# Optimization experiments

Hardware: AMD Instinct MI355X
Metric: run time of the kernel (lower is better)

## Reference

```python
import jax, jax.numpy as jnp
import numpy as np

B, T, D_IN, H, D_OUT = 4096, 512, 10, 20, 2


def setup_inputs() -> dict:
    key = jax.random.key(0)
    ks = jax.random.split(key, 12)
    s = 1.0 / np.sqrt(H)  # PyTorch-style uniform bound scale (use normal*s)
    return {
        "x": jax.random.normal(ks[0], (B, T, D_IN), jnp.float32),
        "w_ih0": jax.random.normal(ks[1], (H, D_IN), jnp.float32) * s,
        "w_hh0": jax.random.normal(ks[2], (H, H), jnp.float32) * s,
        "b_ih0": jax.random.normal(ks[3], (H,), jnp.float32) * s,
        "b_hh0": jax.random.normal(ks[4], (H,), jnp.float32) * s,
        "w_ih1": jax.random.normal(ks[5], (H, H), jnp.float32) * s,
        "w_hh1": jax.random.normal(ks[6], (H, H), jnp.float32) * s,
        "b_ih1": jax.random.normal(ks[7], (H,), jnp.float32) * s,
        "b_hh1": jax.random.normal(ks[8], (H,), jnp.float32) * s,
        "fc_w": jax.random.normal(ks[9], (D_OUT, H), jnp.float32) * s,
        "fc_b": jax.random.normal(ks[10], (D_OUT,), jnp.float32) * s,
    }


def _rnn_layer(inp, w_ih, w_hh, b_ih, b_hh):
    # inp: [B, T, Din]. Precompute input projection once (batched GEMM),
    # then scan the sequential recurrence: h_t = tanh(x_t W_ih^T + b_ih + h_{t-1} W_hh^T + b_hh)
    xp = jnp.einsum('btd,hd->bth', inp, w_ih) + (b_ih + b_hh)  # [B, T, H]

    def step(h, xt):
        h = jnp.tanh(xt + h @ w_hh.T)
        return h, h

    h0 = jnp.zeros((inp.shape[0], w_hh.shape[0]), inp.dtype)
    _, hs = jax.lax.scan(step, h0, jnp.swapaxes(xp, 0, 1))  # hs: [T, B, H]
    return jnp.swapaxes(hs, 0, 1)  # [B, T, H]


def reference(x, w_ih0, w_hh0, b_ih0, b_hh0, w_ih1, w_hh1, b_ih1, b_hh1, fc_w, fc_b):
    h1 = _rnn_layer(x, w_ih0, w_hh0, b_ih0, b_hh0)
    h2 = _rnn_layer(h1, w_ih1, w_hh1, b_ih1, b_hh1)
    last = h2[:, -1, :]  # [B, H]
    return last @ fc_w.T + fc_b  # [B, D_OUT]
```

## Files before the change

### kernel.cpp

```cpp
#include <hip/hip_runtime.h>
#include <cstdint>

constexpr int B_   = 4096;
constexpr int T_   = 512;
constexpr int DIN  = 10;
constexpr int H_   = 20;
constexpr int DOUT = 2;

constexpr int SPW = 3;
constexpr int CH  = 2;
constexpr int XV  = CH * DIN / 4;

typedef float    v2f __attribute__((ext_vector_type(2)));
typedef float    v4f __attribute__((ext_vector_type(4)));
typedef _Float16 h2t __attribute__((ext_vector_type(2)));

__device__ __forceinline__ v2f pkfma(v2f a, v2f b, v2f c) {
    return __builtin_elementwise_fma(a, b, c);
}

__device__ __forceinline__ float fdot2(h2t a, h2t b, float c) {
#if __has_builtin(__builtin_amdgcn_fdot2)
    return __builtin_amdgcn_fdot2(a, b, c, false);
#else
    return fmaf((float)a.x, (float)b.x, fmaf((float)a.y, (float)b.y, c));
#endif
}

__device__ __forceinline__ float fast_tanh(float v) {
    float e = __builtin_amdgcn_exp2f(v * 2.885390082f);
    float r = __builtin_amdgcn_rcpf(e + 1.0f);
    return fmaf(-2.0f, r, 1.0f);
}

union V4H { v4f f; h2t h[4]; };

extern "C" __global__ void __launch_bounds__(64, 1)
rnn_h16(const float* __restrict__ x,
        const float* __restrict__ w_ih0, const float* __restrict__ w_hh0,
        const float* __restrict__ b_ih0, const float* __restrict__ b_hh0,
        const float* __restrict__ w_ih1, const float* __restrict__ w_hh1,
        const float* __restrict__ b_ih1, const float* __restrict__ b_hh1,
        const float* __restrict__ fc_w, const float* __restrict__ fc_b,
        float* __restrict__ out)
{
    const int lane = threadIdx.x;
    const int sl   = lane / H_;
    const int i    = lane - sl * H_;
    const int samp = blockIdx.x * SPW + sl;
    const int sc   = (samp < B_) ? samp : (B_ - 1);
    const int slc  = (sl < SPW) ? sl : SPW;

    __shared__ __align__(16) _Float16 hs[SPW + 1][2 * H_];

    h2t wh0h[10], wi1h[10], wh1h[10];
    {
        const v4f* p0 = reinterpret_cast<const v4f*>(w_hh0 + i * H_);
        const v4f* p1 = reinterpret_cast<const v4f*>(w_ih1 + i * H_);
        const v4f* p2 = reinterpret_cast<const v4f*>(w_hh1 + i * H_);
        #pragma unroll
        for (int k = 0; k < 5; ++k) {
            v4f a = p0[k];
            wh0h[2*k]   = h2t{(_Float16)a.x, (_Float16)a.y};
            wh0h[2*k+1] = h2t{(_Float16)a.z, (_Float16)a.w};
            v4f b = p1[k];
            wi1h[2*k]   = h2t{(_Float16)b.x, (_Float16)b.y};
            wi1h[2*k+1] = h2t{(_Float16)b.z, (_Float16)b.w};
            v4f c = p2[k];
            wh1h[2*k]   = h2t{(_Float16)c.x, (_Float16)c.y};
            wh1h[2*k+1] = h2t{(_Float16)c.z, (_Float16)c.w};
        }
    }
    v2f wi0p[DIN / 2];
    {
        const v2f* p = reinterpret_cast<const v2f*>(w_ih0 + i * DIN);
        #pragma unroll
        for (int k = 0; k < DIN / 2; ++k) wi0p[k] = p[k];
    }
    const float bias0 = b_ih0[i] + b_hh0[i];
    const float bias1 = b_ih1[i] + b_hh1[i];

    h2t h1h[10], h2h[10];
    #pragma unroll
    for (int k = 0; k < 10; ++k) {
        h1h[k] = h2t{(_Float16)0.f, (_Float16)0.f};
        h2h[k] = h2t{(_Float16)0.f, (_Float16)0.f};
    }

    const v4f* xb = reinterpret_cast<const v4f*>(x + (size_t)sc * (T_ * DIN));

    v4f xv[XV];
    #pragma unroll
    for (int k = 0; k < XV; ++k) xv[k] = xb[k];

    auto getpair = [&](int p) -> v2f {
        v4f v = xv[p >> 1];
        return (p & 1) ? (v2f){v.z, v.w} : (v2f){v.x, v.y};
    };

    auto consume_xp = [&](float (&xp)[CH]) {
        #pragma unroll
        for (int m = 0; m < CH; ++m) {
            v2f acc = (v2f){bias0, 0.f};
            #pragma unroll
            for (int q = 0; q < DIN / 2; ++q)
                acc = pkfma(getpair(m * (DIN / 2) + q), wi0p[q], acc);
            xp[m] = acc.x + acc.y;
        }
    };

    auto row_read = [&]() {
        V4H r[5];
        #pragma unroll
        for (int k = 0; k < 5; ++k)
            r[k].f = reinterpret_cast<const v4f*>(&hs[slc][0])[k];
        #pragma unroll
        for (int k = 0; k < 2; ++k) {
            h1h[4*k+0] = r[k].h[0]; h1h[4*k+1] = r[k].h[1];
            h1h[4*k+2] = r[k].h[2]; h1h[4*k+3] = r[k].h[3];
        }
        h1h[8] = r[2].h[0]; h1h[9] = r[2].h[1];
        h2h[0] = r[2].h[2]; h2h[1] = r[2].h[3];
        #pragma unroll
        for (int k = 0; k < 2; ++k) {
            h2h[2+4*k+0] = r[3+k].h[0]; h2h[2+4*k+1] = r[3+k].h[1];
            h2h[2+4*k+2] = r[3+k].h[2]; h2h[2+4*k+3] = r[3+k].h[3];
        }
    };

    auto full_step = [&](float xpm) {
        float a0 = xpm, a1 = 0.f;
        #pragma unroll
        for (int k = 0; k < 5; ++k) {
            a0 = fdot2(h1h[2*k],   wh0h[2*k],   a0);
            a1 = fdot2(h1h[2*k+1], wh0h[2*k+1], a1);
        }
        float h1n = fast_tanh(a0 + a1);

        float b0 = bias1, b1 = 0.f;
        #pragma unroll
        for (int k = 0; k < 5; ++k) {
            b0 = fdot2(h1h[2*k],   wi1h[2*k],   b0);
            b1 = fdot2(h1h[2*k+1], wi1h[2*k+1], b1);
        }
        #pragma unroll
        for (int k = 0; k < 5; ++k) {
            b0 = fdot2(h2h[2*k],   wh1h[2*k],   b0);
            b1 = fdot2(h2h[2*k+1], wh1h[2*k+1], b1);
        }
        float h2n = fast_tanh(b0 + b1);

        hs[slc][i]      = (_Float16)h1n;
        hs[slc][H_ + i] = (_Float16)h2n;
        row_read();
    };

    {
        float xp[CH];
        consume_xp(xp);
        #pragma unroll
        for (int k = 0; k < XV; ++k) xv[k] = xb[(CH * DIN) / 4 + k];

        float h1n = fast_tanh(xp[0]);
        hs[slc][i]      = (_Float16)h1n;
        hs[slc][H_ + i] = (_Float16)0.f;
        row_read();

        #pragma unroll
        for (int m = 1; m < CH; ++m) full_step(xp[m]);
    }

    for (int t0 = CH; t0 < T_; t0 += CH) {
        float xp[CH];
        consume_xp(xp);
        {
            const int t0n = (t0 + CH < T_) ? (t0 + CH) : 0;
            #pragma unroll
            for (int k = 0; k < XV; ++k) xv[k] = xb[(t0n * DIN) / 4 + k];
        }
        #pragma unroll
        for (int m = 0; m < CH; ++m) full_step(xp[m]);
    }

    float h2fin[H_];
    {
        float b0 = bias1, b1 = 0.f;
        #pragma unroll
        for (int k = 0; k < 5; ++k) {
            b0 = fdot2(h1h[2*k],   wi1h[2*k],   b0);
            b1 = fdot2(h1h[2*k+1], wi1h[2*k+1], b1);
        }
        #pragma unroll
        for (int k = 0; k < 5; ++k) {
            b0 = fdot2(h2h[2*k],   wh1h[2*k],   b0);
            b1 = fdot2(h2h[2*k+1], wh1h[2*k+1], b1);
        }
        float h2n = fast_tanh(b0 + b1);
        hs[slc][H_ + i] = (_Float16)h2n;
        #pragma unroll
        for (int j = 0; j < H_; ++j) h2fin[j] = (float)hs[slc][H_ + j];
    }

    if (sl < SPW && samp < B_ && i < DOUT) {
        float acc = fc_b[i];
        #pragma unroll
        for (int j = 0; j < H_; ++j) acc = fmaf(h2fin[j], fc_w[i * H_ + j], acc);
        out[samp * DOUT + i] = acc;
    }
}

extern "C" void kernel_launch(void* const* d_in, const int* in_sizes, int n_in,
                              void* d_out, int out_size, void* d_ws, size_t ws_size,
                              hipStream_t stream) {
    (void)in_sizes; (void)n_in; (void)d_ws; (void)ws_size; (void)out_size;
    const float* x     = (const float*)d_in[0];
    const float* w_ih0 = (const float*)d_in[1];
    const float* w_hh0 = (const float*)d_in[2];
    const float* b_ih0 = (const float*)d_in[3];
    const float* b_hh0 = (const float*)d_in[4];
    const float* w_ih1 = (const float*)d_in[5];
    const float* w_hh1 = (const float*)d_in[6];
    const float* b_ih1 = (const float*)d_in[7];
    const float* b_hh1 = (const float*)d_in[8];
    const float* fc_w  = (const float*)d_in[9];
    const float* fc_b  = (const float*)d_in[10];
    float* out = (float*)d_out;

    const int grid = (B_ + SPW - 1) / SPW;
    hipLaunchKernelGGL(rnn_h16, dim3(grid), dim3(64), 0, stream,
                       x, w_ih0, w_hh0, b_ih0, b_hh0,
                       w_ih1, w_hh1, b_ih1, b_hh1, fc_w, fc_b, out);
}
```

Baseline: 136.7 us.

## Fold tanh scale into weights, split LDS row reads, widen dot accumulators

Pre-multiplies all weights and biases by 2/ln2 so the tanh needs no extra multiply on the serial path. The LDS row is padded to 48 halves so h1 and h2 get separate aligned reads. Layer-0's new h1 is written and read back before the layer-1 dot products run, which overlaps LDS latency with compute. The dependent dot-product chains now use four accumulators instead of two, which shortens the serial latency per step. Scaling the weights before the fp16 conversion slightly changes rounding and the fp16 range used.

```diff
diff --git a/kernel.cpp b/kernel.cpp
--- a/kernel.cpp
+++ b/kernel.cpp
@@ -10,10 +10,13 @@
 constexpr int SPW = 3;
 constexpr int CH  = 2;
 constexpr int XV  = CH * DIN / 4;
+constexpr int RS  = 48;
 
 typedef float    v2f __attribute__((ext_vector_type(2)));
 typedef float    v4f __attribute__((ext_vector_type(4)));
 typedef _Float16 h2t __attribute__((ext_vector_type(2)));
+
+constexpr float SCL = 2.885390082f;
 
 __device__ __forceinline__ v2f pkfma(v2f a, v2f b, v2f c) {
     return __builtin_elementwise_fma(a, b, c);
@@ -27,22 +30,23 @@
 #endif
 }
 
-__device__ __forceinline__ float fast_tanh(float v) {
-    float e = __builtin_amdgcn_exp2f(v * 2.885390082f);
+__device__ __forceinline__ float tanh_pre(float s) {
+    float e = __builtin_amdgcn_exp2f(s);
     float r = __builtin_amdgcn_rcpf(e + 1.0f);
     return fmaf(-2.0f, r, 1.0f);
 }
 
 union V4H { v4f f; h2t h[4]; };
+union V2H { v2f f; h2t h[2]; };
 
 extern "C" __global__ void __launch_bounds__(64, 1)
-rnn_h16(const float* __restrict__ x,
-        const float* __restrict__ w_ih0, const float* __restrict__ w_hh0,
-        const float* __restrict__ b_ih0, const float* __restrict__ b_hh0,
-        const float* __restrict__ w_ih1, const float* __restrict__ w_hh1,
-        const float* __restrict__ b_ih1, const float* __restrict__ b_hh1,
-        const float* __restrict__ fc_w, const float* __restrict__ fc_b,
-        float* __restrict__ out)
+rnn_h16b(const float* __restrict__ x,
+         const float* __restrict__ w_ih0, const float* __restrict__ w_hh0,
+         const float* __restrict__ b_ih0, const float* __restrict__ b_hh0,
+         const float* __restrict__ w_ih1, const float* __restrict__ w_hh1,
+         const float* __restrict__ b_ih1, const float* __restrict__ b_hh1,
+         const float* __restrict__ fc_w, const float* __restrict__ fc_b,
+         float* __restrict__ out)
 {
     const int lane = threadIdx.x;
     const int sl   = lane / H_;
@@ -51,7 +55,8 @@
     const int sc   = (samp < B_) ? samp : (B_ - 1);
     const int slc  = (sl < SPW) ? sl : SPW;
 
-    __shared__ __align__(16) _Float16 hs[SPW + 1][2 * H_];
+    __shared__ __align__(16) _Float16 hs[(SPW + 1) * RS];
+    _Float16* row = &hs[slc * RS];
 
     h2t wh0h[10], wi1h[10], wh1h[10];
     {
@@ -61,24 +66,27 @@
         #pragma unroll
         for (int k = 0; k < 5; ++k) {
             v4f a = p0[k];
-            wh0h[2*k]   = h2t{(_Float16)a.x, (_Float16)a.y};
-            wh0h[2*k+1] = h2t{(_Float16)a.z, (_Float16)a.w};
+            wh0h[2*k]   = h2t{(_Float16)(a.x*SCL), (_Float16)(a.y*SCL)};
+            wh0h[2*k+1] = h2t{(_Float16)(a.z*SCL), (_Float16)(a.w*SCL)};
             v4f b = p1[k];
-            wi1h[2*k]   = h2t{(_Float16)b.x, (_Float16)b.y};
-            wi1h[2*k+1] = h2t{(_Float16)b.z, (_Float16)b.w};
+            wi1h[2*k]   = h2t{(_Float16)(b.x*SCL), (_Float16)(b.y*SCL)};
+            wi1h[2*k+1] = h2t{(_Float16)(b.z*SCL), (_Float16)(b.w*SCL)};
             v4f c = p2[k];
-            wh1h[2*k]   = h2t{(_Float16)c.x, (_Float16)c.y};
-            wh1h[2*k+1] = h2t{(_Float16)c.z, (_Float16)c.w};
+            wh1h[2*k]   = h2t{(_Float16)(c.x*SCL), (_Float16)(c.y*SCL)};
+            wh1h[2*k+1] = h2t{(_Float16)(c.z*SCL), (_Float16)(c.w*SCL)};
         }
     }
     v2f wi0p[DIN / 2];
     {
         const v2f* p = reinterpret_cast<const v2f*>(w_ih0 + i * DIN);
         #pragma unroll
-        for (int k = 0; k < DIN / 2; ++k) wi0p[k] = p[k];
-    }
-    const float bias0 = b_ih0[i] + b_hh0[i];
-    const float bias1 = b_ih1[i] + b_hh1[i];
+        for (int k = 0; k < DIN / 2; ++k) {
+            v2f v = p[k];
+            wi0p[k] = (v2f){v.x * SCL, v.y * SCL};
+        }
+    }
+    const float bias0 = (b_ih0[i] + b_hh0[i]) * SCL;
+    const float bias1 = (b_ih1[i] + b_hh1[i]) * SCL;
 
     h2t h1h[10], h2h[10];
     #pragma unroll
@@ -109,50 +117,66 @@
         }
     };
 
-    auto row_read = [&]() {
-        V4H r[5];
-        #pragma unroll
-        for (int k = 0; k < 5; ++k)
-            r[k].f = reinterpret_cast<const v4f*>(&hs[slc][0])[k];
-        #pragma unroll
-        for (int k = 0; k < 2; ++k) {
-            h1h[4*k+0] = r[k].h[0]; h1h[4*k+1] = r[k].h[1];
-            h1h[4*k+2] = r[k].h[2]; h1h[4*k+3] = r[k].h[3];
-        }
-        h1h[8] = r[2].h[0]; h1h[9] = r[2].h[1];
-        h2h[0] = r[2].h[2]; h2h[1] = r[2].h[3];
-        #pragma unroll
-        for (int k = 0; k < 2; ++k) {
-            h2h[2+4*k+0] = r[3+k].h[0]; h2h[2+4*k+1] = r[3+k].h[1];
-            h2h[2+4*k+2] = r[3+k].h[2]; h2h[2+4*k+3] = r[3+k].h[3];
-        }
+    auto read_h1 = [&](V4H& r0, V4H& r1, V2H& r2) {
+        r0.f = *reinterpret_cast<const v4f*>(row + 0);
+        r1.f = *reinterpret_cast<const v4f*>(row + 8);
+        r2.f = *reinterpret_cast<const v2f*>(row + 16);
+    };
+    auto read_h2 = [&](V4H& r0, V4H& r1, V2H& r2) {
+        r0.f = *reinterpret_cast<const v4f*>(row + 24);
+        r1.f = *reinterpret_cast<const v4f*>(row + 32);
+        r2.f = *reinterpret_cast<const v2f*>(row + 40);
+    };
+    auto commit = [&](h2t (&dst)[10], const V4H& r0, const V4H& r1, const V2H& r2) {
+        dst[0]=r0.h[0]; dst[1]=r0.h[1]; dst[2]=r0.h[2]; dst[3]=r0.h[3];
+        dst[4]=r1.h[0]; dst[5]=r1.h[1]; dst[6]=r1.h[2]; dst[7]=r1.h[3];
+        dst[8]=r2.h[0]; dst[9]=r2.h[1];
     };
 
     auto full_step = [&](float xpm) {
-        float a0 = xpm, a1 = 0.f;
-        #pragma unroll
-        for (int k = 0; k < 5; ++k) {
-            a0 = fdot2(h1h[2*k],   wh0h[2*k],   a0);
-            a1 = fdot2(h1h[2*k+1], wh0h[2*k+1], a1);
-        }
-        float h1n = fast_tanh(a0 + a1);
-
-        float b0 = bias1, b1 = 0.f;
-        #pragma unroll
-        for (int k = 0; k < 5; ++k) {
-            b0 = fdot2(h1h[2*k],   wi1h[2*k],   b0);
-            b1 = fdot2(h1h[2*k+1], wi1h[2*k+1], b1);
-        }
-        #pragma unroll
-        for (int k = 0; k < 5; ++k) {
-            b0 = fdot2(h2h[2*k],   wh1h[2*k],   b0);
-            b1 = fdot2(h2h[2*k+1], wh1h[2*k+1], b1);
-        }
-        float h2n = fast_tanh(b0 + b1);
-
-        hs[slc][i]      = (_Float16)h1n;
-        hs[slc][H_ + i] = (_Float16)h2n;
-        row_read();
+        float a0 = xpm, a1 = 0.f, a2 = 0.f, a3 = 0.f;
+        #pragma unroll
+        for (int k = 0; k < 8; k += 4) {
+            a0 = fdot2(h1h[k+0], wh0h[k+0], a0);
+            a1 = fdot2(h1h[k+1], wh0h[k+1], a1);
+            a2 = fdot2(h1h[k+2], wh0h[k+2], a2);
+            a3 = fdot2(h1h[k+3], wh0h[k+3], a3);
+        }
+        a0 = fdot2(h1h[8], wh0h[8], a0);
+        a1 = fdot2(h1h[9], wh0h[9], a1);
+        float h1n = tanh_pre((a0 + a1) + (a2 + a3));
+
+        row[i] = (_Float16)h1n;
+        V4H n10, n11; V2H n12;
+        read_h1(n10, n11, n12);
+
+        float b0 = bias1, b1 = 0.f, b2 = 0.f, b3 = 0.f;
+        #pragma unroll
+        for (int k = 0; k < 8; k += 4) {
+            b0 = fdot2(h1h[k+0], wi1h[k+0], b0);
+            b1 = fdot2(h1h[k+1], wi1h[k+1], b1);
+            b2 = fdot2(h1h[k+2], wi1h[k+2], b2);
+            b3 = fdot2(h1h[k+3], wi1h[k+3], b3);
+        }
+        b0 = fdot2(h1h[8], wi1h[8], b0);
+        b1 = fdot2(h1h[9], wi1h[9], b1);
+        #pragma unroll
+        for (int k = 0; k < 8; k += 4) {
+            b2 = fdot2(h2h[k+0], wh1h[k+0], b2);
+            b3 = fdot2(h2h[k+1], wh1h[k+1], b3);
+            b0 = fdot2(h2h[k+2], wh1h[k+2], b0);
+            b1 = fdot2(h2h[k+3], wh1h[k+3], b1);
+        }
+        b2 = fdot2(h2h[8], wh1h[8], b2);
+        b3 = fdot2(h2h[9], wh1h[9], b3);
+        float h2n = tanh_pre((b0 + b1) + (b2 + b3));
+
+        row[24 + i] = (_Float16)h2n;
+        V4H n20, n21; V2H n22;
+        read_h2(n20, n21, n22);
+
+        commit(h1h, n10, n11, n12);
+        commit(h2h, n20, n21, n22);
     };
 
     {
@@ -161,10 +185,12 @@
         #pragma unroll
         for (int k = 0; k < XV; ++k) xv[k] = xb[(CH * DIN) / 4 + k];
 
-        float h1n = fast_tanh(xp[0]);
-        hs[slc][i]      = (_Float16)h1n;
-        hs[slc][H_ + i] = (_Float16)0.f;
-        row_read();
+        float h1n = tanh_pre(xp[0]);
+        row[i]      = (_Float16)h1n;
+        row[24 + i] = (_Float16)0.f;
+        V4H n10, n11; V2H n12;
+        read_h1(n10, n11, n12);
+        commit(h1h, n10, n11, n12);
 
         #pragma unroll
         for (int m = 1; m < CH; ++m) full_step(xp[m]);
@@ -184,21 +210,29 @@
 
     float h2fin[H_];
     {
-        float b0 = bias1, b1 = 0.f;
-        #pragma unroll
-        for (int k = 0; k < 5; ++k) {
-            b0 = fdot2(h1h[2*k],   wi1h[2*k],   b0);
-            b1 = fdot2(h1h[2*k+1], wi1h[2*k+1], b1);
-        }
-        #pragma unroll
-        for (int k = 0; k < 5; ++k) {
-            b0 = fdot2(h2h[2*k],   wh1h[2*k],   b0);
-            b1 = fdot2(h2h[2*k+1], wh1h[2*k+1], b1);
-        }
-        float h2n = fast_tanh(b0 + b1);
-        hs[slc][H_ + i] = (_Float16)h2n;
-        #pragma unroll
-        for (int j = 0; j < H_; ++j) h2fin[j] = (float)hs[slc][H_ + j];
+        float b0 = bias1, b1 = 0.f, b2 = 0.f, b3 = 0.f;
+        #pragma unroll
+        for (int k = 0; k < 8; k += 4) {
+            b0 = fdot2(h1h[k+0], wi1h[k+0], b0);
+            b1 = fdot2(h1h[k+1], wi1h[k+1], b1);
+            b2 = fdot2(h1h[k+2], wi1h[k+2], b2);
+            b3 = fdot2(h1h[k+3], wi1h[k+3], b3);
+        }
+        b0 = fdot2(h1h[8], wi1h[8], b0);
+        b1 = fdot2(h1h[9], wi1h[9], b1);
+        #pragma unroll
+        for (int k = 0; k < 8; k += 4) {
+            b2 = fdot2(h2h[k+0], wh1h[k+0], b2);
+            b3 = fdot2(h2h[k+1], wh1h[k+1], b3);
+            b0 = fdot2(h2h[k+2], wh1h[k+2], b0);
+            b1 = fdot2(h2h[k+3], wh1h[k+3], b1);
+        }
+        b2 = fdot2(h2h[8], wh1h[8], b2);
+        b3 = fdot2(h2h[9], wh1h[9], b3);
+        float h2n = tanh_pre((b0 + b1) + (b2 + b3));
+        row[24 + i] = (_Float16)h2n;
+        #pragma unroll
+        for (int j = 0; j < H_; ++j) h2fin[j] = (float)row[24 + j];
     }
 
     if (sl < SPW && samp < B_ && i < DOUT) {
@@ -227,7 +261,7 @@
     float* out = (float*)d_out;
 
     const int grid = (B_ + SPW - 1) / SPW;
-    hipLaunchKernelGGL(rnn_h16, dim3(grid), dim3(64), 0, stream,
+    hipLaunchKernelGGL(rnn_h16b, dim3(grid), dim3(64), 0, stream,
                        x, w_ih0, w_hh0, b_ih0, b_hh0,
                        w_ih1, w_hh1, b_ih1, b_hh1, fc_w, fc_b, out);
 }
```

Measured after the change: 150.0 us. 9.7% more time.
